# Performance work log

Measured on AMD Instinct MI355X. Metric: run time of the kernel, lower is better.

The kernel has to match this reference:

```python
import jax, jax.numpy as jnp
import numpy as np

B, T, IN, H, L, C = 64, 2048, 256, 512, 2, 128


def _uniform(key, shape, bound):
    return jax.random.uniform(key, shape, jnp.float32, -bound, bound)


def setup_inputs() -> dict:
    key = jax.random.key(0)
    ks = jax.random.split(key, 12)
    s = 1.0 / np.sqrt(H)  # PyTorch RNN/Linear init bound
    inp = {
        "x": jax.random.normal(ks[0], (B, T, IN), jnp.float32),
        # layer 0 (input_size -> hidden)
        "W_ih0": _uniform(ks[1], (H, IN), s),
        "W_hh0": _uniform(ks[2], (H, H), s),
        "b_ih0": _uniform(ks[3], (H,), s),
        "b_hh0": _uniform(ks[4], (H,), s),
        # layer 1 (hidden -> hidden)
        "W_ih1": _uniform(ks[5], (H, H), s),
        "W_hh1": _uniform(ks[6], (H, H), s),
        "b_ih1": _uniform(ks[7], (H,), s),
        "b_hh1": _uniform(ks[8], (H,), s),
        # final linear head
        "fc_w": _uniform(ks[9], (C, H), s),
        "fc_b": _uniform(ks[10], (C,), s),
    }
    return inp


def _rnn_layer(x_seq, W_ih, W_hh, b_ih, b_hh):
    """Vanilla ReLU RNN layer: h_t = relu(x_t W_ih^T + b_ih + h_{t-1} W_hh^T + b_hh).
    x_seq: [B, T, D] -> [B, T, H]. Input projection is done as one big GEMM;
    only the recurrent matmul stays inside the scan."""
    pre = jnp.einsum('btd,hd->bth', x_seq, W_ih) + b_ih + b_hh  # [B,T,H]
    h0 = jnp.zeros((x_seq.shape[0], W_hh.shape[0]), x_seq.dtype)

    def step(h, p_t):
        h = jax.nn.relu(p_t + h @ W_hh.T)
        return h, h

    _, hs = jax.lax.scan(step, h0, jnp.swapaxes(pre, 0, 1))  # [T,B,H]
    return jnp.swapaxes(hs, 0, 1)


def reference(x, W_ih0, W_hh0, b_ih0, b_hh0, W_ih1, W_hh1, b_ih1, b_hh1, fc_w, fc_b):
    h = _rnn_layer(x, W_ih0, W_hh0, b_ih0, b_hh0)
    # dropout (rate=0.2) is identity in eval mode -- deterministic reference
    h = _rnn_layer(h, W_ih1, W_hh1, b_ih1, b_hh1)
    last = h[:, -1, :]                 # [B, H]
    return last @ fc_w.T + fc_b        # [B, C]
```

## Files before the change

### kernel.cpp

```cpp
#include <hip/hip_runtime.h>


typedef unsigned short u16;
typedef unsigned int u32;
typedef unsigned long long u64;
typedef _Float16 f16;
typedef _Float16 half8 __attribute__((ext_vector_type(8)));
typedef float float4v __attribute__((ext_vector_type(4)));

#define T_LEN 2048
#define H_DIM 512
#define B_SZ 64
#define SGN 0x8000800080008000ull
#define VMASK 0x7fff7fff7fff7fffull
#define SPIN_LIM (1 << 15)
#define LAG 7

__device__ __forceinline__ float bf2f(u16 u) {
    union { u32 i; float f; } v; v.i = ((u32)u) << 16; return v.f;
}
__device__ __forceinline__ u16 f2bf(float f) {
    u32 x = __float_as_uint(f);
    u32 r = (x + 0x7fffu + ((x >> 16) & 1u)) >> 16;
    return (u16)r;
}
__device__ __forceinline__ float loadf(const void* p, size_t i, int dt) {
    return dt ? ((const float*)p)[i] : bf2f(((const u16*)p)[i]);
}
__device__ __forceinline__ half8 cvt8_bf16(uint4 v) {
    half8 h;
    h[0] = (f16)bf2f((u16)(v.x & 0xffff)); h[1] = (f16)bf2f((u16)(v.x >> 16));
    h[2] = (f16)bf2f((u16)(v.y & 0xffff)); h[3] = (f16)bf2f((u16)(v.y >> 16));
    h[4] = (f16)bf2f((u16)(v.z & 0xffff)); h[5] = (f16)bf2f((u16)(v.z >> 16));
    h[6] = (f16)bf2f((u16)(v.w & 0xffff)); h[7] = (f16)bf2f((u16)(v.w >> 16));
    return h;
}
__device__ __forceinline__ u64 tagmask(int t) {
    return ((t & 1) ? 0x0000000000008000ull : 0ull) |
           ((t & 2) ? 0x0000000080000000ull : 0ull) |
           ((t & 4) ? 0x0000800000000000ull : 0ull) |
           ((t & 8) ? 0x8000000000000000ull : 0ull);
}
__device__ __forceinline__ u64 aload(u64* p) {
    return __hip_atomic_load(p, __ATOMIC_RELAXED, __HIP_MEMORY_SCOPE_AGENT);
}
__device__ __forceinline__ void astore(u64* p, u64 v) {
    __hip_atomic_store(p, v, __ATOMIC_RELAXED, __HIP_MEMORY_SCOPE_AGENT);
}
__device__ __forceinline__ u32 aload32(u32* p) {
    return __hip_atomic_load(p, __ATOMIC_RELAXED, __HIP_MEMORY_SCOPE_AGENT);
}
__device__ __forceinline__ void validate8(u64* src, int rc8, u64 em, u64* vv) {
    int pend = 0;
#pragma unroll
    for (int q = 0; q < 8; ++q)
        if ((vv[q] & SGN) != em) pend |= 1 << q;
    int guard = 0;
    while (pend && guard < SPIN_LIM) {
#pragma unroll
        for (int q = 0; q < 8; ++q)
            if (pend & (1 << q)) vv[q] = aload(&src[rc8 + q]);
#pragma unroll
        for (int q = 0; q < 8; ++q)
            if ((pend & (1 << q)) && ((vv[q] & SGN) == em))
                pend &= ~(1 << q);
        ++guard;
    }
}
__device__ __forceinline__ void validate4i(u64* base, const int* idx, u64 em, u64* vv) {
    int pend = 0;
#pragma unroll
    for (int q = 0; q < 4; ++q)
        if ((vv[q] & SGN) != em) pend |= 1 << q;
    int guard = 0;
    while (pend && guard < SPIN_LIM) {
#pragma unroll
        for (int q = 0; q < 4; ++q)
            if (pend & (1 << q)) vv[q] = aload(&base[idx[q]]);
#pragma unroll
        for (int q = 0; q < 4; ++q)
            if ((pend & (1 << q)) && ((vv[q] & SGN) == em))
                pend &= ~(1 << q);
        ++guard;
    }
}

__global__ void detect_kernel(const u16* __restrict__ xr, int* __restrict__ dtf,
                              u32* __restrict__ progP, u32* __restrict__ progL) {
    int lane = threadIdx.x;
    u16 u0 = xr[(lane * 2 + 0) * 2];
    u16 u1 = xr[(lane * 2 + 1) * 2];
    int e0 = (u0 >> 7) & 0xff, e1 = (u1 >> 7) & 0xff;
    int c0 = (e0 >= 0x60 && e0 <= 0x8f) ? 1 : 0;
    int c1 = (e1 >= 0x60 && e1 <= 0x8f) ? 1 : 0;
    int tot = __popcll(__ballot(c0)) + __popcll(__ballot(c1));
    if (lane == 0) *dtf = (tot >= 96) ? 0 : 1;
    progP[lane] = 0;
    progL[lane] = 0;
}

__global__ void cvt_w_kernel(const void* __restrict__ in, f16* __restrict__ out,
                             int n, const int* __restrict__ dtf) {
    int dt = *dtf;
    for (int i = blockIdx.x * blockDim.x + threadIdx.x; i < n; i += gridDim.x * blockDim.x)
        out[i] = (f16)loadf(in, i, dt);
}

__global__ void bias_kernel(const void* __restrict__ bi, const void* __restrict__ bh,
                            float* __restrict__ bias, const int* __restrict__ dtf) {
    int dt = *dtf;
    int i = blockIdx.x * blockDim.x + threadIdx.x;
    if (i < H_DIM) bias[i] = loadf(bi, i, dt) + loadf(bh, i, dt);
}

__global__ void fcb_kernel(const void* __restrict__ in, float* __restrict__ out,
                           const int* __restrict__ dtf) {
    int i = threadIdx.x;
    if (i < 128) out[i] = loadf(in, i, *dtf);
}

template<int RAW>
__global__ __launch_bounds__(256)
void gemm_tiled(const void* __restrict__ Araw, const f16* __restrict__ Bw,
                const float* __restrict__ bias, f16* __restrict__ C,
                int lgTc, int t_off, int K, const int* __restrict__ dtf)
{
    __shared__ f16 As[64][40];
    __shared__ f16 Bs[64][40];
    const int dt = RAW ? *dtf : 0;
    const int m0 = blockIdx.x * 64, n0 = blockIdx.y * 64;
    const int tid = threadIdx.x;
    const int wv = tid >> 6, lane = tid & 63;
    const int lr = lane & 15, quad = lane >> 4;
    const int srow = tid >> 2, skq = tid & 3;

    float4v acc[4] = {{0.f,0.f,0.f,0.f},{0.f,0.f,0.f,0.f},{0.f,0.f,0.f,0.f},{0.f,0.f,0.f,0.f}};

    size_t arow;
    {
        int ml = m0 + srow;
        if (RAW) {
            int b = ml >> lgTc, tt = ml & ((1 << lgTc) - 1);
            arow = (size_t)b * T_LEN + t_off + tt;
        } else arow = (size_t)ml;
    }
    const f16* pb = Bw + (size_t)(n0 + srow) * K + skq * 8;

    for (int k0 = 0; k0 < K; k0 += 32) {
        half8 av;
        if (RAW) {
            if (dt) {
                const float* ap = (const float*)Araw + arow * K + k0 + skq * 8;
                float4v f0 = *(const float4v*)ap;
                float4v f1 = *(const float4v*)(ap + 4);
                av[0]=(f16)f0[0]; av[1]=(f16)f0[1]; av[2]=(f16)f0[2]; av[3]=(f16)f0[3];
                av[4]=(f16)f1[0]; av[5]=(f16)f1[1]; av[6]=(f16)f1[2]; av[7]=(f16)f1[3];
            } else {
                av = cvt8_bf16(*(const uint4*)((const u16*)Araw + arow * K + k0 + skq * 8));
            }
        } else {
            av = *(const half8*)((const f16*)Araw + arow * K + k0 + skq * 8);
        }
        half8 bv = *(const half8*)(pb + k0);
        __syncthreads();
        *(half8*)&As[srow][skq * 8] = av;
        *(half8*)&Bs[srow][skq * 8] = bv;
        __syncthreads();
        half8 bf = *(const half8*)&Bs[wv * 16 + lr][quad * 8];
#pragma unroll
        for (int mt = 0; mt < 4; ++mt) {
            half8 af = *(const half8*)&As[mt * 16 + lr][quad * 8];
            acc[mt] = __builtin_amdgcn_mfma_f32_16x16x32_f16(af, bf, acc[mt], 0, 0, 0);
        }
    }
    const int n = n0 + wv * 16 + lr;
    const float bval = bias[n];
#pragma unroll
    for (int mt = 0; mt < 4; ++mt) {
#pragma unroll
        for (int i = 0; i < 4; ++i) {
            int m = m0 + mt * 16 + quad * 4 + i;
            C[(size_t)m * H_DIM + n] = (f16)(acc[mt][i] + bval);
        }
    }
}

__global__ __launch_bounds__(256, 1)
void rnn_fused_scan(const f16* __restrict__ pre0,
                    const f16* __restrict__ Whh0,
                    const f16* __restrict__ Wih1,
                    const f16* __restrict__ Whh1,
                    const float* __restrict__ bias1,
                    u64* __restrict__ hex0,
                    u64* __restrict__ hex1,
                    u64* __restrict__ hexZ,
                    f16* __restrict__ hc0,
                    f16* __restrict__ hc1,
                    u32* __restrict__ progP,
                    u32* __restrict__ progL,
                    int t0, int Tc,
                    float* __restrict__ h_last)
{
    __shared__ f16 stage[2][16 * 512];
    __shared__ f16 sH0[16 * 512];
    const int b = blockIdx.x;
    int role, r, cg;
    if (b < 32) { int c = b & 7; role = c >> 2; r = c & 3; cg = b >> 3; }
    else        { role = 2; r = (b - 32) >> 2; cg = (b - 32) & 3; }
    const int rows0 = r * 16;
    const int tid = threadIdx.x;
    const int w = tid >> 6, lane = tid & 63;
    const int lr = lane & 15, quad = lane >> 4;
    const int c0w = cg * 128 + w * 32;
    const int rrow = tid >> 4;
    const int rc8 = (tid & 15) * 8;
    const bool mine = ((tid & 15) >> 2) == cg;

    if (role == 2) {
        half8 BfI[2][16];
#pragma unroll
        for (int j = 0; j < 2; ++j)
#pragma unroll
            for (int kc = 0; kc < 16; ++kc)
                BfI[j][kc] = *(const half8*)(Wih1 + (size_t)(c0w + j * 16 + lr) * H_DIM
                                             + kc * 32 + quad * 8);
        float bvv[2] = { bias1[c0w + lr], bias1[c0w + 16 + lr] };
        const int lc0 = w * 32 + lr, lc1 = lc0 + 16;

        u64 vv[8];
        {
            u64* src = hex0 + ((size_t)(t0 & 7) * 64 + rows0 + rrow) * 128;
#pragma unroll
            for (int q = 0; q < 8; ++q) vv[q] = aload(&src[rc8 + q]);
        }

        for (int tt = 0; tt < Tc; ++tt) {
            const int t = t0 + tt;
            const int nb = t & 7;
            const u64 em = tagmask(t);
            const int need = t - LAG;
            const u32 want = (u32)(need + 1);

            u32 plv = 0xffffffffu;
            if (need >= 0) plv = aload32(&progL[r * 16 + cg]);

            {
                u64* src = hex0 + ((size_t)nb * 64 + rows0 + rrow) * 128;
                validate8(src, rc8, em, vv);
#pragma unroll
                for (int q = 0; q < 8; ++q) {
                    int cu = rc8 + q;
                    *(u64*)&sH0[rrow * 512 + ((cu >> 1) ^ (rrow & 7)) * 8 + (cu & 1) * 4] =
                        vv[q] & VMASK;
                }
            }
            __syncthreads();
            if (tid == 0)
                __hip_atomic_store(&progP[r * 16 + cg], (u32)(t + 1), __ATOMIC_RELAXED,
                                   __HIP_MEMORY_SCOPE_AGENT);

            float4v acc0 = {0.f,0.f,0.f,0.f}, acc1 = {0.f,0.f,0.f,0.f};
#pragma unroll
            for (int kc = 0; kc < 16; ++kc) {
                half8 a = *(const half8*)&sH0[lr * 512 + (((kc * 4 + quad) ^ (lr & 7)) * 8)];
                acc0 = __builtin_amdgcn_mfma_f32_16x16x32_f16(a, BfI[0][kc], acc0, 0, 0, 0);
                acc1 = __builtin_amdgcn_mfma_f32_16x16x32_f16(a, BfI[1][kc], acc1, 0, 0, 0);
            }

            u64 zw[4];
#pragma unroll
            for (int j = 0; j < 2; ++j) {
                const float4v& a = j ? acc1 : acc0;
                u64 wp = 0, wn = 0;
#pragma unroll
                for (int i = 0; i < 4; ++i) {
                    float z = a[i] + bvv[j];
                    union { f16 h; u16 u; } cp, cn;
                    cp.h = (f16)fmaxf(z, 0.f);
                    cn.h = (f16)fmaxf(-z, 0.f);
                    wp |= ((u64)cp.u) << (16 * i);
                    wn |= ((u64)cn.u) << (16 * i);
                }
                zw[j] = wp; zw[2 + j] = wn;
            }
            __syncthreads();

            if (need >= 0) {
                int g = 0;
                while (plv < want && g < SPIN_LIM) {
                    plv = aload32(&progL[r * 16 + cg]);
                    ++g;
                }
            }

            {
                u64* dz = hexZ + ((((size_t)nb * 4 + r) * 4 + cg) * 1024);
                astore(&dz[lc0 * 4 + quad],        zw[0] | em);
                astore(&dz[lc1 * 4 + quad],        zw[1] | em);
                astore(&dz[512 + lc0 * 4 + quad],  zw[2] | em);
                astore(&dz[512 + lc1 * 4 + quad],  zw[3] | em);
            }
            if (tt + 1 < Tc) {
                u64* srcn = hex0 + ((size_t)((t + 1) & 7) * 64 + rows0 + rrow) * 128;
#pragma unroll
                for (int q = 0; q < 8; ++q) vv[q] = aload(&srcn[rc8 + q]);
            }
        }
        return;
    }

    const f16* Wrec = (role == 0) ? Whh0 : Whh1;
    half8 Bf[2][16];
#pragma unroll
    for (int j = 0; j < 2; ++j)
#pragma unroll
        for (int kc = 0; kc < 16; ++kc)
            Bf[j][kc] = *(const half8*)(Wrec + (size_t)(c0w + j * 16 + lr) * H_DIM
                                        + kc * 32 + quad * 8);
    f16* hcarry = (role == 0) ? hc0 : hc1;
    u64* hexOwn = (role == 0) ? hex0 : hex1;

    if (t0 > 0) {
        int row = tid >> 4, g0 = (tid & 15) * 4;
#pragma unroll
        for (int gq = 0; gq < 4; ++gq) {
            int g = g0 + gq;
            *(uint4*)&stage[(t0 - 1) & 1][row * 512 + ((g ^ (row & 7)) * 8)] =
                *(const uint4*)(hcarry + (size_t)(rows0 + row) * H_DIM + g * 8);
        }
    }
    __syncthreads();

    u64 sv[8];
    float pv[2][4];
    u64 vvz[4];
    int idxz[4];
    const int lc0 = w * 32 + lr, lc1 = lc0 + 16;
    idxz[0] = lc0 * 4 + quad;       idxz[1] = lc1 * 4 + quad;
    idxz[2] = 512 + lc0 * 4 + quad; idxz[3] = 512 + lc1 * 4 + quad;

    if (role == 0) {
#pragma unroll
        for (int j = 0; j < 2; ++j)
#pragma unroll
            for (int i = 0; i < 4; ++i)
                pv[j][i] = (float)pre0[((size_t)(rows0 + quad * 4 + i) * Tc + 0) * H_DIM
                                       + c0w + j * 16 + lr];
    } else {
        u64* zb = hexZ + ((((size_t)(t0 & 7) * 4 + r) * 4 + cg) * 1024);
#pragma unroll
        for (int q = 0; q < 4; ++q) vvz[q] = aload(&zb[idxz[q]]);
    }

    for (int tt = 0; tt < Tc; ++tt) {
        const int t = t0 + tt;
        const int p = (t - 1) & 1, np = t & 1;
        const u64 em = tagmask(t);
        const int nbOwn = (role == 0) ? (t & 7) : (t & 1);
        const int need = t - LAG;
        const u32 want = (u32)(need + 1);

        u32 ppv = 0xffffffffu;
        if (role == 0 && need >= 0 && lane < 4)
            ppv = aload32(&progP[r * 16 + lane]);

        if (tt > 0 && !mine) {
            u64* src;
            if (role == 0)
                src = hex0 + ((size_t)((t - 1) & 7) * 64 + rows0 + rrow) * 128;
            else
                src = hex1 + ((size_t)((t - 1) & 1) * 64 + rows0 + rrow) * 128;
            validate8(src, rc8, tagmask(t - 1), sv);
#pragma unroll
            for (int q = 0; q < 8; ++q) {
                int cu = rc8 + q;
                *(u64*)&stage[p][rrow * 512 + ((cu >> 1) ^ (rrow & 7)) * 8 + (cu & 1) * 4] =
                    sv[q] & VMASK;
            }
        }
        __syncthreads();

        float4v acc0 = {0.f,0.f,0.f,0.f}, acc1 = {0.f,0.f,0.f,0.f};
        if (t > 0) {
            const f16* sb = stage[p];
#pragma unroll
            for (int kc = 0; kc < 16; ++kc) {
                half8 a = *(const half8*)&sb[lr * 512 + (((kc * 4 + quad) ^ (lr & 7)) * 8)];
                acc0 = __builtin_amdgcn_mfma_f32_16x16x32_f16(a, Bf[0][kc], acc0, 0, 0, 0);
                acc1 = __builtin_amdgcn_mfma_f32_16x16x32_f16(a, Bf[1][kc], acc1, 0, 0, 0);
            }
        }

        if (role == 1) {
            u64* zb = hexZ + ((((size_t)(t & 7) * 4 + r) * 4 + cg) * 1024);
            validate4i(zb, idxz, em, vvz);
            if (tid == 0)
                __hip_atomic_store(&progL[r * 16 + cg], (u32)(t + 1), __ATOMIC_RELAXED,
                                   __HIP_MEMORY_SCOPE_AGENT);
#pragma unroll
            for (int j = 0; j < 2; ++j) {
                u64 pw = vvz[j] & VMASK, nw = vvz[2 + j] & VMASK;
#pragma unroll
                for (int i = 0; i < 4; ++i) {
                    union { u16 u; f16 h; } cp, cn;
                    cp.u = (u16)(pw >> (16 * i));
                    cn.u = (u16)(nw >> (16 * i));
                    pv[j][i] = (float)cp.h - (float)cn.h;
                }
            }
        }

        f16* swp = stage[np];
        f16 hv16[2][4];
#pragma unroll
        for (int j = 0; j < 2; ++j) {
            const float4v& a = j ? acc1 : acc0;
#pragma unroll
            for (int i = 0; i < 4; ++i) {
                float hval = fmaxf(a[i] + pv[j][i], 0.f);
                hv16[j][i] = (f16)hval;
                int row = quad * 4 + i, lc = c0w + j * 16 + lr;
                swp[row * 512 + ((lc >> 3) ^ (row & 7)) * 8 + (lc & 7)] = hv16[j][i];
            }
        }
        if (role == 1 && h_last && t == T_LEN - 1) {
#pragma unroll
            for (int j = 0; j < 2; ++j)
#pragma unroll
                for (int i = 0; i < 4; ++i)
                    h_last[(size_t)(rows0 + quad * 4 + i) * H_DIM + c0w + j * 16 + lr] =
                        (float)hv16[j][i];
        }
        if (tt == Tc - 1) {
#pragma unroll
            for (int j = 0; j < 2; ++j)
#pragma unroll
                for (int i = 0; i < 4; ++i)
                    hcarry[(size_t)(rows0 + quad * 4 + i) * H_DIM + c0w + j * 16 + lr] =
                        hv16[j][i];
        }
        __syncthreads();

        if (role == 0 && need >= 0) {
            bool ok = __all((lane < 4) ? (ppv >= want) : 1);
            int g = 0;
            while (!ok && g < SPIN_LIM) {
                if (lane < 4) ppv = aload32(&progP[r * 16 + lane]);
                ok = __all((lane < 4) ? (ppv >= want) : 1);
                ++g;
            }
        }

        {
            int row = tid >> 4, poc = (tid & 15) * 2, cu = cg * 32 + poc;
            uint4 q4 = *(const uint4*)&stage[np][row * 512 + (((cu >> 1) ^ (row & 7)) * 8)];
            u64 v0 = (((u64)q4.y) << 32) | q4.x;
            u64 v1 = (((u64)q4.w) << 32) | q4.z;
            u64* dst = hexOwn + ((size_t)nbOwn * 64 + rows0 + row) * 128;
            astore(&dst[cu], v0 | em);
            astore(&dst[cu + 1], v1 | em);
        }
        if (!mine) {
            u64* src = hexOwn + ((size_t)nbOwn * 64 + rows0 + rrow) * 128;
#pragma unroll
            for (int q = 0; q < 8; ++q) sv[q] = aload(&src[rc8 + q]);
        }
        if (tt + 1 < Tc) {
            if (role == 0) {
#pragma unroll
                for (int j = 0; j < 2; ++j)
#pragma unroll
                    for (int i = 0; i < 4; ++i)
                        pv[j][i] = (float)pre0[((size_t)(rows0 + quad * 4 + i) * Tc + tt + 1)
                                               * H_DIM + c0w + j * 16 + lr];
            } else {
                u64* zb = hexZ + ((((size_t)((t + 1) & 7) * 4 + r) * 4 + cg) * 1024);
#pragma unroll
                for (int q = 0; q < 4; ++q) vvz[q] = aload(&zb[idxz[q]]);
            }
        }
    }
}

__global__ void fc_kernel(const float* __restrict__ hlast, const f16* __restrict__ fcw,
                          const float* __restrict__ fcb, void* __restrict__ out,
                          const int* __restrict__ dtf) {
    int b = blockIdx.x, c = threadIdx.x;
    const float* hrow = hlast + b * H_DIM;
    const f16* wrow = fcw + (size_t)c * H_DIM;
    float s = fcb[c];
    for (int h0 = 0; h0 < H_DIM; h0 += 8) {
        half8 w = *(const half8*)(wrow + h0);
#pragma unroll
        for (int j = 0; j < 8; ++j) s += hrow[h0 + j] * (float)w[j];
    }
    if (*dtf) ((float*)out)[b * 128 + c] = s;
    else      ((u16*)out)[b * 128 + c] = f2bf(s);
}

extern "C" void kernel_launch(void* const* d_in, const int* in_sizes, int n_in,
                              void* d_out, int out_size, void* d_ws, size_t ws_size,
                              hipStream_t stream)
{
    const void* x     = d_in[0];
    const void* W_ih0 = d_in[1];
    const void* W_hh0 = d_in[2];
    const void* b_ih0 = d_in[3];
    const void* b_hh0 = d_in[4];
    const void* W_ih1 = d_in[5];
    const void* W_hh1 = d_in[6];
    const void* b_ih1 = d_in[7];
    const void* b_hh1 = d_in[8];
    const void* fc_w  = d_in[9];
    const void* fc_b  = d_in[10];

    char* ws = (char*)d_ws;
    int*   dtf   = (int*)(ws + 0);
    float* bias0 = (float*)(ws + 4096);
    float* bias1 = (float*)(ws + 6144);
    float* fcbf  = (float*)(ws + 8192);
    u32*   progP = (u32*)(ws + 12288);
    u32*   progL = (u32*)(ws + 12544);
    float* hlast = (float*)(ws + 16384);
    f16*   hc0   = (f16*)(ws + 147456);
    f16*   hc1   = (f16*)(ws + 212992);
    u64*   hex0  = (u64*)(ws + 278528);
    u64*   hex1  = (u64*)(ws + 802816);
    u64*   hexZ  = (u64*)(ws + 933888);
    f16*   Wih0f = (f16*)(ws + 1982464);
    f16*   Whh0f = (f16*)(ws + 2244608);
    f16*   Wih1f = (f16*)(ws + 2768896);
    f16*   Whh1f = (f16*)(ws + 3293184);
    f16*   fcwf  = (f16*)(ws + 3817472);

    const size_t misc = 4u << 20;
    int Tc = 128;
    {
        auto need = [&](int tc) {
            return misc + (size_t)B_SZ * (size_t)tc * H_DIM * 2;
        };
        if (ws_size >= need(2048)) Tc = 2048;
        else if (ws_size >= need(1024)) Tc = 1024;
        else if (ws_size >= need(512)) Tc = 512;
        else if (ws_size >= need(256)) Tc = 256;
        else Tc = 128;
    }
    int lgTc = 31 - __builtin_clz((unsigned)Tc);
    f16* bufA = (f16*)(ws + misc);

    detect_kernel<<<dim3(1), dim3(64), 0, stream>>>((const u16*)x, dtf, progP, progL);
    cvt_w_kernel<<<dim3(512), dim3(256), 0, stream>>>(W_ih0, Wih0f, H_DIM * 256, dtf);
    cvt_w_kernel<<<dim3(1024), dim3(256), 0, stream>>>(W_hh0, Whh0f, H_DIM * H_DIM, dtf);
    cvt_w_kernel<<<dim3(1024), dim3(256), 0, stream>>>(W_ih1, Wih1f, H_DIM * H_DIM, dtf);
    cvt_w_kernel<<<dim3(1024), dim3(256), 0, stream>>>(W_hh1, Whh1f, H_DIM * H_DIM, dtf);
    cvt_w_kernel<<<dim3(256), dim3(256), 0, stream>>>(fc_w, fcwf, 128 * H_DIM, dtf);
    bias_kernel<<<dim3(2), dim3(256), 0, stream>>>(b_ih0, b_hh0, bias0, dtf);
    bias_kernel<<<dim3(2), dim3(256), 0, stream>>>(b_ih1, b_hh1, bias1, dtf);
    fcb_kernel<<<dim3(1), dim3(128), 0, stream>>>(fc_b, fcbf, dtf);

    const int NC = T_LEN / Tc;
    const int mblocks = B_SZ * Tc / 64;
    for (int c = 0; c < NC; ++c) {
        const int t0 = c * Tc;
        gemm_tiled<1><<<dim3(mblocks, 8), 256, 0, stream>>>(
            x, Wih0f, bias0, bufA, lgTc, t0, 256, dtf);
        rnn_fused_scan<<<dim3(48), 256, 0, stream>>>(
            bufA, Whh0f, Wih1f, Whh1f, bias1, hex0, hex1, hexZ, hc0, hc1,
            progP, progL, t0, Tc, hlast);
    }
    fc_kernel<<<dim3(B_SZ), dim3(128), 0, stream>>>(hlast, fcwf, fcbf, d_out, dtf);
}
```

Before: 7.716 ms.

## Give each recurrent layer one 512-thread block per batch slice, removing hex1 exchange

The fused scan is reworked from 48 blocks of 256 threads, where four column-group blocks per batch slice exchanged hidden state through global memory each step, to 16 blocks of 512 threads. Each recurrent block now owns all 512 hidden columns for its 16 rows, so the step-to-step hidden state stays in shared memory and the hex1 exchange buffer is gone. Each layer-1 input projection block covers half the columns instead of a quarter. Each thread holds half of its weight slice in registers and streams the other half from global memory every step, which adds load latency and memory traffic to the serial critical path. The per-step work per block doubles while cross-block synchronisation shrinks.

```diff
diff --git a/kernel.cpp b/kernel.cpp
--- a/kernel.cpp
+++ b/kernel.cpp
@@ -50,35 +50,25 @@
 __device__ __forceinline__ u32 aload32(u32* p) {
     return __hip_atomic_load(p, __ATOMIC_RELAXED, __HIP_MEMORY_SCOPE_AGENT);
 }
-__device__ __forceinline__ void validate8(u64* src, int rc8, u64 em, u64* vv) {
+__device__ __forceinline__ void astore32(u32* p, u32 v) {
+    __hip_atomic_store(p, v, __ATOMIC_RELAXED, __HIP_MEMORY_SCOPE_AGENT);
+}
+__device__ __forceinline__ float f16u(u16 b) {
+    union { u16 u; f16 h; } c; c.u = b; return (float)c.h;
+}
+template<int N>
+__device__ __forceinline__ void validateN(u64* base, const int* idx, u64 em, u64* vv) {
     int pend = 0;
 #pragma unroll
-    for (int q = 0; q < 8; ++q)
+    for (int q = 0; q < N; ++q)
         if ((vv[q] & SGN) != em) pend |= 1 << q;
     int guard = 0;
     while (pend && guard < SPIN_LIM) {
 #pragma unroll
-        for (int q = 0; q < 8; ++q)
-            if (pend & (1 << q)) vv[q] = aload(&src[rc8 + q]);
-#pragma unroll
-        for (int q = 0; q < 8; ++q)
-            if ((pend & (1 << q)) && ((vv[q] & SGN) == em))
-                pend &= ~(1 << q);
-        ++guard;
-    }
-}
-__device__ __forceinline__ void validate4i(u64* base, const int* idx, u64 em, u64* vv) {
-    int pend = 0;
-#pragma unroll
-    for (int q = 0; q < 4; ++q)
-        if ((vv[q] & SGN) != em) pend |= 1 << q;
-    int guard = 0;
-    while (pend && guard < SPIN_LIM) {
-#pragma unroll
-        for (int q = 0; q < 4; ++q)
+        for (int q = 0; q < N; ++q)
             if (pend & (1 << q)) vv[q] = aload(&base[idx[q]]);
 #pragma unroll
-        for (int q = 0; q < 4; ++q)
+        for (int q = 0; q < N; ++q)
             if ((pend & (1 << q)) && ((vv[q] & SGN) == em))
                 pend &= ~(1 << q);
         ++guard;
@@ -185,53 +175,52 @@
     }
 }
 
-__global__ __launch_bounds__(256, 1)
-void rnn_fused_scan(const f16* __restrict__ pre0,
-                    const f16* __restrict__ Whh0,
-                    const f16* __restrict__ Wih1,
-                    const f16* __restrict__ Whh1,
-                    const float* __restrict__ bias1,
-                    u64* __restrict__ hex0,
-                    u64* __restrict__ hex1,
-                    u64* __restrict__ hexZ,
-                    f16* __restrict__ hc0,
-                    f16* __restrict__ hc1,
-                    u32* __restrict__ progP,
-                    u32* __restrict__ progL,
-                    int t0, int Tc,
-                    float* __restrict__ h_last)
+__global__ __launch_bounds__(512, 2)
+void rnn_scan3(const f16* __restrict__ pre0,
+               const f16* __restrict__ Whh0,
+               const f16* __restrict__ Wih1,
+               const f16* __restrict__ Whh1,
+               const float* __restrict__ bias1,
+               u64* __restrict__ hex0,
+               u64* __restrict__ hexZ,
+               f16* __restrict__ hc0,
+               f16* __restrict__ hc1,
+               u32* __restrict__ progP,
+               u32* __restrict__ progL,
+               int t0, int Tc,
+               float* __restrict__ h_last)
 {
-    __shared__ f16 stage[2][16 * 512];
+    __shared__ f16 stage[16 * 512];
     __shared__ f16 sH0[16 * 512];
-    const int b = blockIdx.x;
-    int role, r, cg;
-    if (b < 32) { int c = b & 7; role = c >> 2; r = c & 3; cg = b >> 3; }
-    else        { role = 2; r = (b - 32) >> 2; cg = (b - 32) & 3; }
-    const int rows0 = r * 16;
+    const int bid = blockIdx.x;
     const int tid = threadIdx.x;
     const int w = tid >> 6, lane = tid & 63;
     const int lr = lane & 15, quad = lane >> 4;
-    const int c0w = cg * 128 + w * 32;
-    const int rrow = tid >> 4;
-    const int rc8 = (tid & 15) * 8;
-    const bool mine = ((tid & 15) >> 2) == cg;
-
-    if (role == 2) {
-        half8 BfI[2][16];
+
+    if (bid >= 8) {
+        const int r = (bid - 8) >> 1, half = (bid - 8) & 1;
+        const int rows0 = r * 16;
+        const int c0p = half * 256 + w * 32;
+        half8 Bf[2][16];
 #pragma unroll
         for (int j = 0; j < 2; ++j)
 #pragma unroll
             for (int kc = 0; kc < 16; ++kc)
-                BfI[j][kc] = *(const half8*)(Wih1 + (size_t)(c0w + j * 16 + lr) * H_DIM
-                                             + kc * 32 + quad * 8);
-        float bvv[2] = { bias1[c0w + lr], bias1[c0w + 16 + lr] };
+                Bf[j][kc] = *(const half8*)(Wih1 + (size_t)(c0p + j * 16 + lr) * H_DIM
+                                            + kc * 32 + quad * 8);
+        float bvv[2] = { bias1[c0p + lr], bias1[c0p + 16 + lr] };
+        const int rrow = tid >> 5;
+        const int rc4 = (tid & 31) * 4;
+        int hidx[4];
+#pragma unroll
+        for (int q = 0; q < 4; ++q) hidx[q] = rc4 + q;
         const int lc0 = w * 32 + lr, lc1 = lc0 + 16;
 
-        u64 vv[8];
+        u64 vv[4];
         {
             u64* src = hex0 + ((size_t)(t0 & 7) * 64 + rows0 + rrow) * 128;
 #pragma unroll
-            for (int q = 0; q < 8; ++q) vv[q] = aload(&src[rc8 + q]);
+            for (int q = 0; q < 4; ++q) vv[q] = aload(&src[hidx[q]]);
         }
 
         for (int tt = 0; tt < Tc; ++tt) {
@@ -242,29 +231,27 @@
             const u32 want = (u32)(need + 1);
 
             u32 plv = 0xffffffffu;
-            if (need >= 0) plv = aload32(&progL[r * 16 + cg]);
+            if (need >= 0) plv = aload32(&progL[r]);
 
             {
                 u64* src = hex0 + ((size_t)nb * 64 + rows0 + rrow) * 128;
-                validate8(src, rc8, em, vv);
-#pragma unroll
-                for (int q = 0; q < 8; ++q) {
-                    int cu = rc8 + q;
+                validateN<4>(src, hidx, em, vv);
+#pragma unroll
+                for (int q = 0; q < 4; ++q) {
+                    int cu = rc4 + q;
                     *(u64*)&sH0[rrow * 512 + ((cu >> 1) ^ (rrow & 7)) * 8 + (cu & 1) * 4] =
                         vv[q] & VMASK;
                 }
             }
             __syncthreads();
-            if (tid == 0)
-                __hip_atomic_store(&progP[r * 16 + cg], (u32)(t + 1), __ATOMIC_RELAXED,
-                                   __HIP_MEMORY_SCOPE_AGENT);
+            if (tid == 0) astore32(&progP[r * 2 + half], (u32)(t + 1));
 
             float4v acc0 = {0.f,0.f,0.f,0.f}, acc1 = {0.f,0.f,0.f,0.f};
 #pragma unroll
             for (int kc = 0; kc < 16; ++kc) {
                 half8 a = *(const half8*)&sH0[lr * 512 + (((kc * 4 + quad) ^ (lr & 7)) * 8)];
-                acc0 = __builtin_amdgcn_mfma_f32_16x16x32_f16(a, BfI[0][kc], acc0, 0, 0, 0);
-                acc1 = __builtin_amdgcn_mfma_f32_16x16x32_f16(a, BfI[1][kc], acc1, 0, 0, 0);
+                acc0 = __builtin_amdgcn_mfma_f32_16x16x32_f16(a, Bf[0][kc], acc0, 0, 0, 0);
+                acc1 = __builtin_amdgcn_mfma_f32_16x16x32_f16(a, Bf[1][kc], acc1, 0, 0, 0);
             }
 
             u64 zw[4];
@@ -283,33 +270,36 @@
                 }
                 zw[j] = wp; zw[2 + j] = wn;
             }
-            __syncthreads();
 
             if (need >= 0) {
                 int g = 0;
-                while (plv < want && g < SPIN_LIM) {
-                    plv = aload32(&progL[r * 16 + cg]);
-                    ++g;
-                }
+                while (plv < want && g < SPIN_LIM) { plv = aload32(&progL[r]); ++g; }
             }
 
             {
-                u64* dz = hexZ + ((((size_t)nb * 4 + r) * 4 + cg) * 1024);
+                u64* dz = hexZ + (((size_t)nb * 4 + r) * 2 + half) * 2048;
                 astore(&dz[lc0 * 4 + quad],        zw[0] | em);
                 astore(&dz[lc1 * 4 + quad],        zw[1] | em);
-                astore(&dz[512 + lc0 * 4 + quad],  zw[2] | em);
-                astore(&dz[512 + lc1 * 4 + quad],  zw[3] | em);
+                astore(&dz[1024 + lc0 * 4 + quad], zw[2] | em);
+                astore(&dz[1024 + lc1 * 4 + quad], zw[3] | em);
             }
             if (tt + 1 < Tc) {
                 u64* srcn = hex0 + ((size_t)((t + 1) & 7) * 64 + rows0 + rrow) * 128;
 #pragma unroll
-                for (int q = 0; q < 8; ++q) vv[q] = aload(&srcn[rc8 + q]);
-            }
+                for (int q = 0; q < 4; ++q) vv[q] = aload(&srcn[hidx[q]]);
+            }
+            __syncthreads();
         }
         return;
     }
 
-    const f16* Wrec = (role == 0) ? Whh0 : Whh1;
+    const int role = bid >> 2;
+    const int r = bid & 3;
+    const int rows0 = r * 16;
+    const int c0w = w * 64;
+    const f16* Wrec = role ? Whh1 : Whh0;
+    f16* hcar = role ? hc1 : hc0;
+
     half8 Bf[2][16];
 #pragma unroll
     for (int j = 0; j < 2; ++j)
@@ -317,166 +307,153 @@
         for (int kc = 0; kc < 16; ++kc)
             Bf[j][kc] = *(const half8*)(Wrec + (size_t)(c0w + j * 16 + lr) * H_DIM
                                         + kc * 32 + quad * 8);
-    f16* hcarry = (role == 0) ? hc0 : hc1;
-    u64* hexOwn = (role == 0) ? hex0 : hex1;
+    const f16* Wg2 = Wrec + (size_t)(c0w + 32 + lr) * H_DIM + quad * 8;
+    const f16* Wg3 = Wrec + (size_t)(c0w + 48 + lr) * H_DIM + quad * 8;
 
     if (t0 > 0) {
-        int row = tid >> 4, g0 = (tid & 15) * 4;
-#pragma unroll
-        for (int gq = 0; gq < 4; ++gq) {
+        int row = tid >> 5, g0 = (tid & 31) * 2;
+#pragma unroll
+        for (int gq = 0; gq < 2; ++gq) {
             int g = g0 + gq;
-            *(uint4*)&stage[(t0 - 1) & 1][row * 512 + ((g ^ (row & 7)) * 8)] =
-                *(const uint4*)(hcarry + (size_t)(rows0 + row) * H_DIM + g * 8);
+            *(uint4*)&stage[row * 512 + ((g ^ (row & 7)) * 8)] =
+                *(const uint4*)(hcar + (size_t)(rows0 + row) * H_DIM + g * 8);
         }
     }
     __syncthreads();
 
-    u64 sv[8];
-    float pv[2][4];
-    u64 vvz[4];
-    int idxz[4];
-    const int lc0 = w * 32 + lr, lc1 = lc0 + 16;
-    idxz[0] = lc0 * 4 + quad;       idxz[1] = lc1 * 4 + quad;
-    idxz[2] = 512 + lc0 * 4 + quad; idxz[3] = 512 + lc1 * 4 + quad;
-
-    if (role == 0) {
-#pragma unroll
-        for (int j = 0; j < 2; ++j)
+    u64 vvz[8];
+    int zidx[8];
+    const int halfW = w >> 2, lcw = (w & 3) * 64;
+    if (role) {
+#pragma unroll
+        for (int j = 0; j < 4; ++j) {
+            zidx[j] = (lcw + j * 16 + lr) * 4 + quad;
+            zidx[4 + j] = 1024 + zidx[j];
+        }
+        u64* zb = hexZ + (((size_t)(t0 & 7) * 4 + r) * 2 + halfW) * 2048;
+#pragma unroll
+        for (int q = 0; q < 8; ++q) vvz[q] = aload(&zb[zidx[q]]);
+    }
+
+    float pv[4][4];
+    if (!role) {
+#pragma unroll
+        for (int j = 0; j < 4; ++j)
 #pragma unroll
             for (int i = 0; i < 4; ++i)
                 pv[j][i] = (float)pre0[((size_t)(rows0 + quad * 4 + i) * Tc + 0) * H_DIM
                                        + c0w + j * 16 + lr];
-    } else {
-        u64* zb = hexZ + ((((size_t)(t0 & 7) * 4 + r) * 4 + cg) * 1024);
-#pragma unroll
-        for (int q = 0; q < 4; ++q) vvz[q] = aload(&zb[idxz[q]]);
-    }
+    }
+
+    const int prow = tid >> 5, pc4 = (tid & 31) * 4;
 
     for (int tt = 0; tt < Tc; ++tt) {
         const int t = t0 + tt;
-        const int p = (t - 1) & 1, np = t & 1;
+        const int nb = t & 7;
         const u64 em = tagmask(t);
-        const int nbOwn = (role == 0) ? (t & 7) : (t & 1);
         const int need = t - LAG;
         const u32 want = (u32)(need + 1);
 
         u32 ppv = 0xffffffffu;
-        if (role == 0 && need >= 0 && lane < 4)
-            ppv = aload32(&progP[r * 16 + lane]);
-
-        if (tt > 0 && !mine) {
-            u64* src;
-            if (role == 0)
-                src = hex0 + ((size_t)((t - 1) & 7) * 64 + rows0 + rrow) * 128;
-            else
-                src = hex1 + ((size_t)((t - 1) & 1) * 64 + rows0 + rrow) * 128;
-            validate8(src, rc8, tagmask(t - 1), sv);
-#pragma unroll
-            for (int q = 0; q < 8; ++q) {
-                int cu = rc8 + q;
-                *(u64*)&stage[p][rrow * 512 + ((cu >> 1) ^ (rrow & 7)) * 8 + (cu & 1) * 4] =
-                    sv[q] & VMASK;
+        if (!role && need >= 0 && lane < 2)
+            ppv = aload32(&progP[r * 2 + lane]);
+
+        float4v acc[4] = {{0.f,0.f,0.f,0.f},{0.f,0.f,0.f,0.f},
+                          {0.f,0.f,0.f,0.f},{0.f,0.f,0.f,0.f}};
+        if (t > 0) {
+            half8 w2[4], w3[4];
+#pragma unroll
+            for (int kk = 0; kk < 4; ++kk) {
+                w2[kk] = *(const half8*)(Wg2 + kk * 32);
+                w3[kk] = *(const half8*)(Wg3 + kk * 32);
+            }
+#pragma unroll
+            for (int kc = 0; kc < 16; ++kc) {
+                half8 a = *(const half8*)&stage[lr * 512 + (((kc * 4 + quad) ^ (lr & 7)) * 8)];
+                acc[0] = __builtin_amdgcn_mfma_f32_16x16x32_f16(a, Bf[0][kc], acc[0], 0, 0, 0);
+                acc[1] = __builtin_amdgcn_mfma_f32_16x16x32_f16(a, Bf[1][kc], acc[1], 0, 0, 0);
+                acc[2] = __builtin_amdgcn_mfma_f32_16x16x32_f16(a, w2[kc & 3], acc[2], 0, 0, 0);
+                acc[3] = __builtin_amdgcn_mfma_f32_16x16x32_f16(a, w3[kc & 3], acc[3], 0, 0, 0);
+                if (kc < 12) {
+                    w2[kc & 3] = *(const half8*)(Wg2 + (kc + 4) * 32);
+                    w3[kc & 3] = *(const half8*)(Wg3 + (kc + 4) * 32);
+                }
+            }
+        }
+
+        if (role) {
+            u64* zb = hexZ + (((size_t)nb * 4 + r) * 2 + halfW) * 2048;
+            validateN<8>(zb, zidx, em, vvz);
+#pragma unroll
+            for (int j = 0; j < 4; ++j) {
+                u64 pw = vvz[j] & VMASK, nw = vvz[4 + j] & VMASK;
+#pragma unroll
+                for (int i = 0; i < 4; ++i)
+                    pv[j][i] = f16u((u16)(pw >> (16 * i))) - f16u((u16)(nw >> (16 * i)));
             }
         }
         __syncthreads();
-
-        float4v acc0 = {0.f,0.f,0.f,0.f}, acc1 = {0.f,0.f,0.f,0.f};
-        if (t > 0) {
-            const f16* sb = stage[p];
-#pragma unroll
-            for (int kc = 0; kc < 16; ++kc) {
-                half8 a = *(const half8*)&sb[lr * 512 + (((kc * 4 + quad) ^ (lr & 7)) * 8)];
-                acc0 = __builtin_amdgcn_mfma_f32_16x16x32_f16(a, Bf[0][kc], acc0, 0, 0, 0);
-                acc1 = __builtin_amdgcn_mfma_f32_16x16x32_f16(a, Bf[1][kc], acc1, 0, 0, 0);
-            }
-        }
-
-        if (role == 1) {
-            u64* zb = hexZ + ((((size_t)(t & 7) * 4 + r) * 4 + cg) * 1024);
-            validate4i(zb, idxz, em, vvz);
-            if (tid == 0)
-                __hip_atomic_store(&progL[r * 16 + cg], (u32)(t + 1), __ATOMIC_RELAXED,
-                                   __HIP_MEMORY_SCOPE_AGENT);
-#pragma unroll
-            for (int j = 0; j < 2; ++j) {
-                u64 pw = vvz[j] & VMASK, nw = vvz[2 + j] & VMASK;
-#pragma unroll
-                for (int i = 0; i < 4; ++i) {
-                    union { u16 u; f16 h; } cp, cn;
-                    cp.u = (u16)(pw >> (16 * i));
-                    cn.u = (u16)(nw >> (16 * i));
-                    pv[j][i] = (float)cp.h - (float)cn.h;
-                }
-            }
-        }
-
-        f16* swp = stage[np];
-        f16 hv16[2][4];
-#pragma unroll
-        for (int j = 0; j < 2; ++j) {
-            const float4v& a = j ? acc1 : acc0;
+        if (role && tid == 0) astore32(&progL[r], (u32)(t + 1));
+
+        f16 hv[4][4];
+#pragma unroll
+        for (int j = 0; j < 4; ++j)
 #pragma unroll
             for (int i = 0; i < 4; ++i) {
-                float hval = fmaxf(a[i] + pv[j][i], 0.f);
-                hv16[j][i] = (f16)hval;
+                float hval = fmaxf(acc[j][i] + pv[j][i], 0.f);
+                hv[j][i] = (f16)hval;
                 int row = quad * 4 + i, lc = c0w + j * 16 + lr;
-                swp[row * 512 + ((lc >> 3) ^ (row & 7)) * 8 + (lc & 7)] = hv16[j][i];
-            }
-        }
-        if (role == 1 && h_last && t == T_LEN - 1) {
-#pragma unroll
-            for (int j = 0; j < 2; ++j)
+                stage[row * 512 + ((lc >> 3) ^ (row & 7)) * 8 + (lc & 7)] = hv[j][i];
+            }
+        if (role && h_last && t == T_LEN - 1) {
+#pragma unroll
+            for (int j = 0; j < 4; ++j)
 #pragma unroll
                 for (int i = 0; i < 4; ++i)
                     h_last[(size_t)(rows0 + quad * 4 + i) * H_DIM + c0w + j * 16 + lr] =
-                        (float)hv16[j][i];
+                        (float)hv[j][i];
         }
         if (tt == Tc - 1) {
 #pragma unroll
-            for (int j = 0; j < 2; ++j)
+            for (int j = 0; j < 4; ++j)
 #pragma unroll
                 for (int i = 0; i < 4; ++i)
-                    hcarry[(size_t)(rows0 + quad * 4 + i) * H_DIM + c0w + j * 16 + lr] =
-                        hv16[j][i];
+                    hcar[(size_t)(rows0 + quad * 4 + i) * H_DIM + c0w + j * 16 + lr] =
+                        hv[j][i];
         }
         __syncthreads();
 
-        if (role == 0 && need >= 0) {
-            bool ok = __all((lane < 4) ? (ppv >= want) : 1);
-            int g = 0;
-            while (!ok && g < SPIN_LIM) {
-                if (lane < 4) ppv = aload32(&progP[r * 16 + lane]);
-                ok = __all((lane < 4) ? (ppv >= want) : 1);
-                ++g;
-            }
-        }
-
-        {
-            int row = tid >> 4, poc = (tid & 15) * 2, cu = cg * 32 + poc;
-            uint4 q4 = *(const uint4*)&stage[np][row * 512 + (((cu >> 1) ^ (row & 7)) * 8)];
-            u64 v0 = (((u64)q4.y) << 32) | q4.x;
-            u64 v1 = (((u64)q4.w) << 32) | q4.z;
-            u64* dst = hexOwn + ((size_t)nbOwn * 64 + rows0 + row) * 128;
-            astore(&dst[cu], v0 | em);
-            astore(&dst[cu + 1], v1 | em);
-        }
-        if (!mine) {
-            u64* src = hexOwn + ((size_t)nbOwn * 64 + rows0 + rrow) * 128;
-#pragma unroll
-            for (int q = 0; q < 8; ++q) sv[q] = aload(&src[rc8 + q]);
-        }
-        if (tt + 1 < Tc) {
-            if (role == 0) {
-#pragma unroll
-                for (int j = 0; j < 2; ++j)
+        if (!role) {
+            if (need >= 0) {
+                bool ok = __all((lane < 2) ? (ppv >= want) : 1);
+                int g = 0;
+                while (!ok && g < SPIN_LIM) {
+                    if (lane < 2) ppv = aload32(&progP[r * 2 + lane]);
+                    ok = __all((lane < 2) ? (ppv >= want) : 1);
+                    ++g;
+                }
+            }
+            u64* dst = hex0 + ((size_t)nb * 64 + rows0 + prow) * 128;
+#pragma unroll
+            for (int q = 0; q < 4; ++q) {
+                int cu = pc4 + q;
+                u64 v = *(const u64*)&stage[prow * 512 + ((cu >> 1) ^ (prow & 7)) * 8
+                                            + (cu & 1) * 4];
+                astore(&dst[cu], v | em);
+            }
+            if (tt + 1 < Tc) {
+#pragma unroll
+                for (int j = 0; j < 4; ++j)
 #pragma unroll
                     for (int i = 0; i < 4; ++i)
                         pv[j][i] = (float)pre0[((size_t)(rows0 + quad * 4 + i) * Tc + tt + 1)
                                                * H_DIM + c0w + j * 16 + lr];
-            } else {
-                u64* zb = hexZ + ((((size_t)((t + 1) & 7) * 4 + r) * 4 + cg) * 1024);
-#pragma unroll
-                for (int q = 0; q < 4; ++q) vvz[q] = aload(&zb[idxz[q]]);
+            }
+        } else {
+            if (tt + 1 < Tc) {
+                u64* zb = hexZ + (((size_t)((t + 1) & 7) * 4 + r) * 2 + halfW) * 2048;
+#pragma unroll
+                for (int q = 0; q < 8; ++q) vvz[q] = aload(&zb[zidx[q]]);
             }
         }
     }
@@ -525,13 +502,12 @@
     f16*   hc0   = (f16*)(ws + 147456);
     f16*   hc1   = (f16*)(ws + 212992);
     u64*   hex0  = (u64*)(ws + 278528);
-    u64*   hex1  = (u64*)(ws + 802816);
-    u64*   hexZ  = (u64*)(ws + 933888);
-    f16*   Wih0f = (f16*)(ws + 1982464);
-    f16*   Whh0f = (f16*)(ws + 2244608);
-    f16*   Wih1f = (f16*)(ws + 2768896);
-    f16*   Whh1f = (f16*)(ws + 3293184);
-    f16*   fcwf  = (f16*)(ws + 3817472);
+    u64*   hexZ  = (u64*)(ws + 802816);
+    f16*   Wih0f = (f16*)(ws + 1851392);
+    f16*   Whh0f = (f16*)(ws + 2113536);
+    f16*   Wih1f = (f16*)(ws + 2637824);
+    f16*   Whh1f = (f16*)(ws + 3162112);
+    f16*   fcwf  = (f16*)(ws + 3686400);
 
     const size_t misc = 4u << 20;
     int Tc = 128;
@@ -564,8 +540,8 @@
         const int t0 = c * Tc;
         gemm_tiled<1><<<dim3(mblocks, 8), 256, 0, stream>>>(
             x, Wih0f, bias0, bufA, lgTc, t0, 256, dtf);
-        rnn_fused_scan<<<dim3(48), 256, 0, stream>>>(
-            bufA, Whh0f, Wih1f, Whh1f, bias1, hex0, hex1, hexZ, hc0, hc1,
+        rnn_scan3<<<dim3(16), dim3(512), 0, stream>>>(
+            bufA, Whh0f, Wih1f, Whh1f, bias1, hex0, hexZ, hc0, hc1,
             progP, progL, t0, Tc, hlast);
     }
     fc_kernel<<<dim3(B_SZ), dim3(128), 0, stream>>>(hlast, fcwf, fcbf, d_out, dtf);
```

After: 23.22 ms. 3.01x slower.
